# Optimization experiments

Hardware: AMD Instinct MI355X
Metric: run time of the kernel (lower is better)

The kernel has to match this reference:

```python
import jax, jax.numpy as jnp
import numpy as np

T, B, D, H = 2048, 64, 512, 512

def setup_inputs() -> dict:
    key = jax.random.key(0)
    ks = jax.random.split(key, 5)
    scale = 1.0 / np.sqrt(D + H)  # ~ torch Linear init scale
    inputs = jax.random.normal(ks[0], (T, B, D), dtype=jnp.float32)
    Wf = jax.random.normal(ks[1], (D + H, H), dtype=jnp.float32) * scale
    Wi = jax.random.normal(ks[2], (D + H, H), dtype=jnp.float32) * scale
    Wg = jax.random.normal(ks[3], (D + H, H), dtype=jnp.float32) * scale
    Wo = jax.random.normal(ks[4], (D + H, H), dtype=jnp.float32) * scale
    z = jnp.zeros((H,), dtype=jnp.float32)
    return {"inputs": inputs, "Wf": Wf, "bf": z, "Wi": Wi, "bi": z,
            "Wg": Wg, "bg": z, "Wo": Wo, "bo": z}

def reference(inputs, Wf, bf, Wi, bi, Wg, bg, Wo, bo):
    # Fuse the 4 gate GEMMs into one [D+H, 4H] matmul per step (same math).
    W = jnp.concatenate([Wf, Wi, Wg, Wo], axis=1)          # [D+H, 4H]
    b = jnp.concatenate([bf, bi, bg, bo], axis=0)          # [4H]
    Hdim = Wf.shape[1]
    Bsz = inputs.shape[1]
    h0 = jnp.zeros((Bsz, Hdim), dtype=inputs.dtype)
    c0 = jnp.zeros((Bsz, Hdim), dtype=inputs.dtype)

    def step(carry, x):
        hx, cx = carry
        combined = jnp.concatenate([x, hx], axis=1)        # [B, D+H]
        gates = combined @ W + b                           # [B, 4H]
        f, i, g, o = jnp.split(gates, 4, axis=1)
        f = jax.nn.sigmoid(f)
        i = jax.nn.sigmoid(i)
        g = jnp.tanh(g)
        o = jax.nn.sigmoid(o)
        cx = f * cx + i * g
        hx = o * jnp.tanh(cx)
        return (hx, cx), hx

    (hT, cT), stacked = jax.lax.scan(step, (h0, c0), inputs)
    return stacked, (hT, cT)
```

## Files before the change

### kernel.cpp

```cpp
#include <hip/hip_runtime.h>
#include <hip/hip_bf16.h>


#define T_N 2048
#define B_N 64
#define D_N 512
#define H_N 512
#define NBLK 64
#define NHEAT 192
#define CPB 8
#define GCPB 32
#define NTHR 256

#define STACK_ELEMS ((size_t)T_N * B_N * H_N)
#define HT_OFF STACK_ELEMS
#define CT_OFF (STACK_ELEMS + (size_t)B_N * H_N)

#define WS_DONE 0
#define WS_FLAGS 1024
#define WS_MIRROR 32768
#define WS_XB 262144

typedef __attribute__((ext_vector_type(4))) float f32x4;
typedef __attribute__((ext_vector_type(8))) short bf16x8;

__device__ __forceinline__ unsigned short f2bf(float f) {
  union { __hip_bfloat16 h; unsigned short u; } u;
  u.h = __float2bfloat16(f);
  return u.u;
}
__device__ __forceinline__ float bf2f(unsigned short us) {
  union { unsigned u32; float f; } x;
  x.u32 = ((unsigned)us) << 16;
  return x.f;
}
__device__ __forceinline__ float sigf(float x) { return 1.0f / (1.0f + __expf(-x)); }
__device__ __forceinline__ float tanhfast(float x) { return 1.0f - 2.0f / (__expf(2.0f * x) + 1.0f); }

__global__ void init_ws_kernel(unsigned* ws32) {
  int i = blockIdx.x * blockDim.x + threadIdx.x;
  if (i < 65536) ws32[i] = 0u;
}

__global__ void xconv_kernel(const float* __restrict__ X, unsigned short* __restrict__ Xb) {
  size_t i = ((size_t)blockIdx.x * blockDim.x + threadIdx.x) * 8;
  float4 v0 = *(const float4*)(X + i);
  float4 v1 = *(const float4*)(X + i + 4);
  bf16x8 o;
  o[0] = (short)f2bf(v0.x); o[1] = (short)f2bf(v0.y);
  o[2] = (short)f2bf(v0.z); o[3] = (short)f2bf(v0.w);
  o[4] = (short)f2bf(v1.x); o[5] = (short)f2bf(v1.y);
  o[6] = (short)f2bf(v1.z); o[7] = (short)f2bf(v1.w);
  *(bf16x8*)(Xb + i) = o;
}

__device__ __forceinline__ void load_x_tile(const unsigned short* Xb, const float* X,
                                            int t, int arow, int kg, bf16x8 (&xa)[16]) {
  if (Xb) {
    const unsigned short* xp = Xb + ((size_t)t * B_N + arow) * D_N + kg;
#pragma unroll
    for (int kk = 0; kk < 16; ++kk) xa[kk] = *(const bf16x8*)(xp + kk * 32);
  } else {
    const float* xp = X + ((size_t)t * B_N + arow) * D_N + kg;
#pragma unroll
    for (int kk = 0; kk < 16; ++kk) {
      float4 v0 = *(const float4*)(xp + kk * 32);
      float4 v1 = *(const float4*)(xp + kk * 32 + 4);
      bf16x8 a;
      a[0] = (short)f2bf(v0.x); a[1] = (short)f2bf(v0.y);
      a[2] = (short)f2bf(v0.z); a[3] = (short)f2bf(v0.w);
      a[4] = (short)f2bf(v1.x); a[5] = (short)f2bf(v1.y);
      a[6] = (short)f2bf(v1.z); a[7] = (short)f2bf(v1.w);
      xa[kk] = a;
    }
  }
}

__global__ __launch_bounds__(NTHR, 1) void lstm_kernel(
    const float* __restrict__ X, const unsigned short* __restrict__ Xb,
    const float* __restrict__ Wf, const float* __restrict__ bF,
    const float* __restrict__ Wi, const float* __restrict__ bI,
    const float* __restrict__ Wg, const float* __restrict__ bG,
    const float* __restrict__ Wo, const float* __restrict__ bO,
    unsigned char* wsb, float* __restrict__ out) {
  __shared__ unsigned short Wl[GCPB * (D_N + H_N)];
  __shared__ unsigned sReady;
  __shared__ int hstop;

  const int tid = threadIdx.x;
  const int blk = blockIdx.x;
  const int lane = tid & 63;

  if (blk >= NBLK) {
    if (tid == 0) *(volatile int*)&hstop = 0;
    __syncthreads();
    const unsigned* dp = (const unsigned*)(wsb + WS_DONE);
    float a = 1.0f + (float)(blk * NTHR + tid) * 1e-7f;
    const float hm = 0.99993f, hc = 1e-8f;
    for (long i = 0;; ++i) {
#pragma unroll
      for (int j = 0; j < 512; ++j) a = __builtin_fmaf(a, hm, hc);
      if (tid == 0 && (i & 63) == 0) {
        unsigned d = __hip_atomic_load(dp, __ATOMIC_RELAXED, __HIP_MEMORY_SCOPE_AGENT);
        if (d >= (unsigned)NBLK) *(volatile int*)&hstop = 1;
      }
      if (*(volatile int*)&hstop) break;
      if (i > (1l << 21)) break;
    }
    asm volatile("" :: "v"(a));
    return;
  }

  const int c0 = blk * CPB;
  const int w = tid >> 6;
  const int l16 = lane & 15;
  const int g16 = lane >> 4;
  const int cc = l16 & 7;
  const bool lo = (l16 < 8);

  if (tid == 0) *(volatile unsigned*)&sReady = 0u;

  for (int idx = tid; idx < GCPB * (D_N + H_N); idx += NTHR) {
    int k = idx >> 5;
    int cl = idx & 31;
    const float* wsrc = (cl < 8) ? Wf : (cl < 16) ? Wi : (cl < 24) ? Wg : Wo;
    float v = wsrc[(size_t)k * H_N + c0 + (cl & 7)];
    int pos = ((k >> 5) * 1024) + ((cl >> 4) * 512) + (((k >> 3) & 3) * 128) + ((cl & 15) * 8) + (k & 7);
    Wl[pos] = f2bf(v);
  }
  const float bias0 = lo ? bF[c0 + cc] : bI[c0 + cc];
  const float bias1 = lo ? bG[c0 + cc] : bO[c0 + cc];
  __syncthreads();

  const int arow = 16 * w + l16;
  const int kg = 8 * g16;
  const int lofs8 = lane * 8;
  const bool owner = (arow == blk);

  bf16x8 wb0[32], wb1[32];
#pragma unroll
  for (int K = 0; K < 32; ++K) {
    wb0[K] = *(const bf16x8*)&Wl[K * 1024 + lofs8];
    wb1[K] = *(const bf16x8*)&Wl[K * 1024 + 512 + lofs8];
  }

  unsigned* flags = (unsigned*)(wsb + WS_FLAGS);
  float cst[4] = {0.f, 0.f, 0.f, 0.f};
  float hT_local[4] = {0.f, 0.f, 0.f, 0.f};

  bf16x8 xa[16];
  load_x_tile(Xb, X, 0, arow, kg, xa);

  for (int t = 0; t < T_N; ++t) {
    const int slotR = (t + 1) & 1;
    const int slotW = t & 1;

    f32x4 x0a = {0,0,0,0}, x0b = {0,0,0,0}, x1a = {0,0,0,0}, x1b = {0,0,0,0};
#pragma unroll
    for (int kk = 0; kk < 8; ++kk) {
      x0a = __builtin_amdgcn_mfma_f32_16x16x32_bf16(xa[kk], wb0[kk], x0a, 0, 0, 0);
      x1a = __builtin_amdgcn_mfma_f32_16x16x32_bf16(xa[kk], wb1[kk], x1a, 0, 0, 0);
    }
#pragma unroll
    for (int kk = 8; kk < 16; ++kk) {
      x0b = __builtin_amdgcn_mfma_f32_16x16x32_bf16(xa[kk], wb0[kk], x0b, 0, 0, 0);
      x1b = __builtin_amdgcn_mfma_f32_16x16x32_bf16(xa[kk], wb1[kk], x1b, 0, 0, 0);
    }

    if (t > 0) {
      const unsigned tgt = (unsigned)t;
      if (w == 0) {
        long guard = 0;
        for (;;) {
          unsigned fv = __hip_atomic_load(flags + lane, __ATOMIC_RELAXED, __HIP_MEMORY_SCOPE_AGENT);
          if (__all((int)(fv >= tgt))) break;
          if (++guard > 2) __builtin_amdgcn_s_sleep(8);
          if (guard > (1l << 16)) break;
        }
        if (lane == 0) *(volatile unsigned*)&sReady = tgt;
      } else {
        long guard = 0;
        while (*(volatile unsigned*)&sReady < tgt) {
          if (++guard > (1l << 22)) break;
        }
      }
    }

    unsigned long long hq0[16], hq1[16];
    {
      const unsigned long long* hbase =
          (const unsigned long long*)(wsb + WS_MIRROR + (size_t)slotR * 65536);
#pragma unroll
      for (int kk = 0; kk < 16; ++kk) {
        const unsigned long long* hp = hbase + (size_t)(g16 + 4 * kk) * 128 + arow * 2;
        hq0[kk] = __hip_atomic_load(hp, __ATOMIC_RELAXED, __HIP_MEMORY_SCOPE_AGENT);
        hq1[kk] = __hip_atomic_load(hp + 1, __ATOMIC_RELAXED, __HIP_MEMORY_SCOPE_AGENT);
      }
    }

    f32x4 h0a = {0,0,0,0}, h0b = {0,0,0,0}, h1a = {0,0,0,0}, h1b = {0,0,0,0};
#pragma unroll
    for (int kk = 0; kk < 8; ++kk) {
      union { unsigned long long q[2]; bf16x8 v; } u;
      u.q[0] = hq0[kk]; u.q[1] = hq1[kk];
      h0a = __builtin_amdgcn_mfma_f32_16x16x32_bf16(u.v, wb0[16 + kk], h0a, 0, 0, 0);
      h1a = __builtin_amdgcn_mfma_f32_16x16x32_bf16(u.v, wb1[16 + kk], h1a, 0, 0, 0);
    }
#pragma unroll
    for (int kk = 8; kk < 16; ++kk) {
      union { unsigned long long q[2]; bf16x8 v; } u;
      u.q[0] = hq0[kk]; u.q[1] = hq1[kk];
      h0b = __builtin_amdgcn_mfma_f32_16x16x32_bf16(u.v, wb0[16 + kk], h0b, 0, 0, 0);
      h1b = __builtin_amdgcn_mfma_f32_16x16x32_bf16(u.v, wb1[16 + kk], h1b, 0, 0, 0);
    }
    f32x4 m0v = (x0a + x0b) + (h0a + h0b);
    f32x4 m1v = (x1a + x1b) + (h1a + h1b);

    float hv[4];
#pragma unroll
    for (int r = 0; r < 4; ++r) {
      float m0 = m0v[r] + bias0;
      float m1 = m1v[r] + bias1;
      float p0 = __shfl_xor(m0, 8, 64);
      float p1 = __shfl_xor(m1, 8, 64);
      float fv = lo ? m0 : p0;
      float iv = lo ? p0 : m0;
      float gv = lo ? m1 : p1;
      float ov = lo ? p1 : m1;
      float f = sigf(fv), i = sigf(iv), g = tanhfast(gv), o = sigf(ov);
      float c = f * cst[r] + i * g;
      cst[r] = c;
      hv[r] = o * tanhfast(c);
    }

    {
      unsigned* rb = (unsigned*)(wsb + WS_MIRROR + (size_t)slotW * 65536) + blk * 256;
#pragma unroll
      for (int r = 0; r < 4; ++r) {
        int row = 16 * w + 4 * g16 + r;
        unsigned short hb = f2bf(hv[r]);
        unsigned opp = __shfl_xor((unsigned)hb, 1, 64);
        if (lo && (cc & 1) == 0) {
          unsigned pack = (unsigned)hb | (opp << 16);
          __hip_atomic_store(rb + row * 4 + (cc >> 1), pack,
                             __ATOMIC_RELAXED, __HIP_MEMORY_SCOPE_AGENT);
        }
      }
    }

    asm volatile("s_waitcnt vmcnt(0)" ::: "memory");
    __syncthreads();
    if (tid == 0) {
      __hip_atomic_store(flags + blk, (unsigned)(t + 1),
                         __ATOMIC_RELAXED, __HIP_MEMORY_SCOPE_AGENT);
    }

    if (t + 1 < T_N) load_x_tile(Xb, X, t + 1, arow, kg, xa);

    if (owner && t > 0) {
      float* oprev = out + (size_t)(t - 1) * (B_N * H_N) + (size_t)blk * H_N + kg;
#pragma unroll
      for (int kk = 0; kk < 16; ++kk) {
        union { unsigned long long q[2]; bf16x8 v; } u;
        u.q[0] = hq0[kk]; u.q[1] = hq1[kk];
        float4 f0, f1;
        f0.x = bf2f((unsigned short)u.v[0]); f0.y = bf2f((unsigned short)u.v[1]);
        f0.z = bf2f((unsigned short)u.v[2]); f0.w = bf2f((unsigned short)u.v[3]);
        f1.x = bf2f((unsigned short)u.v[4]); f1.y = bf2f((unsigned short)u.v[5]);
        f1.z = bf2f((unsigned short)u.v[6]); f1.w = bf2f((unsigned short)u.v[7]);
        *(float4*)(oprev + kk * 32) = f0;
        *(float4*)(oprev + kk * 32 + 4) = f1;
      }
    }

    if (t == T_N - 1) {
      float* obase = out + (size_t)t * (B_N * H_N);
#pragma unroll
      for (int r = 0; r < 4; ++r) {
        int row = 16 * w + 4 * g16 + r;
        if (lo) obase[(size_t)row * H_N + c0 + cc] = hv[r];
        hT_local[r] = hv[r];
      }
    }
  }

  if (lo) {
#pragma unroll
    for (int r = 0; r < 4; ++r) {
      int row = 16 * w + 4 * g16 + r;
      out[HT_OFF + (size_t)row * H_N + c0 + cc] = hT_local[r];
      out[CT_OFF + (size_t)row * H_N + c0 + cc] = cst[r];
    }
  }
  __syncthreads();
  if (tid == 0)
    __hip_atomic_fetch_add((unsigned*)(wsb + WS_DONE), 1u,
                           __ATOMIC_RELAXED, __HIP_MEMORY_SCOPE_AGENT);
}

extern "C" void kernel_launch(void* const* d_in, const int* in_sizes, int n_in,
                              void* d_out, int out_size, void* d_ws, size_t ws_size,
                              hipStream_t stream) {
  const float* X  = (const float*)d_in[0];
  const float* Wf = (const float*)d_in[1];
  const float* bF = (const float*)d_in[2];
  const float* Wi = (const float*)d_in[3];
  const float* bI = (const float*)d_in[4];
  const float* Wg = (const float*)d_in[5];
  const float* bG = (const float*)d_in[6];
  const float* Wo = (const float*)d_in[7];
  const float* bO = (const float*)d_in[8];
  float* out = (float*)d_out;

  unsigned char* ws = (unsigned char*)d_ws;
  const size_t need_xb = WS_XB + (size_t)T_N * B_N * D_N * 2;
  unsigned short* Xb = (ws_size >= need_xb) ? (unsigned short*)(ws + WS_XB) : nullptr;

  init_ws_kernel<<<dim3(256), dim3(256), 0, stream>>>((unsigned*)ws);
  if (Xb) {
    xconv_kernel<<<dim3((T_N * B_N * D_N) / 8 / 256), dim3(256), 0, stream>>>(X, Xb);
  }
  lstm_kernel<<<dim3(NBLK + NHEAT), dim3(NTHR), 0, stream>>>(
      X, Xb, Wf, bF, Wi, bI, Wg, bG, Wo, bO, ws, out);
}
```

Baseline: 10.72 ms.

## Halve persistent LSTM blocks to 32 with 512 threads covering two column slices

Each persistent block now runs 8 waves split into two 8-column gate slices, so only 32 blocks take part in the per-step all-to-all flag barrier instead of 64. The hidden-state exchange buffer is relaid as a per-block 16-column ring with matching read addressing, and the output-owner mapping is adjusted to match. The spin-wait sleeps are shortened and the guard limits raised. Fewer participants should cut barrier latency per timestep, at the cost of doubling per-CU register and MFMA work per block and adding more intra-block synchronisation.

Result: slower. 38.03 ms (+254.9%).

```diff
diff --git a/kernel.cpp b/kernel.cpp
--- a/kernel.cpp
+++ b/kernel.cpp
@@ -6,11 +6,10 @@
 #define B_N 64
 #define D_N 512
 #define H_N 512
-#define NBLK 64
-#define NHEAT 192
-#define CPB 8
-#define GCPB 32
-#define NTHR 256
+#define NBLK 32
+#define NHEAT 224
+#define NTHR 512
+#define BH (B_N * H_N)
 
 #define STACK_ELEMS ((size_t)T_N * B_N * H_N)
 #define HT_OFF STACK_ELEMS
@@ -18,7 +17,7 @@
 
 #define WS_DONE 0
 #define WS_FLAGS 1024
-#define WS_MIRROR 32768
+#define WS_RING 32768
 #define WS_XB 262144
 
 typedef __attribute__((ext_vector_type(4))) float f32x4;
@@ -83,7 +82,7 @@
     const float* __restrict__ Wg, const float* __restrict__ bG,
     const float* __restrict__ Wo, const float* __restrict__ bO,
     unsigned char* wsb, float* __restrict__ out) {
-  __shared__ unsigned short Wl[GCPB * (D_N + H_N)];
+  __shared__ unsigned short Wl[32768];
   __shared__ unsigned sReady;
   __shared__ int hstop;
 
@@ -111,8 +110,9 @@
     return;
   }
 
-  const int c0 = blk * CPB;
   const int w = tid >> 6;
+  const int cs = w >> 2;
+  const int m = w & 3;
   const int l16 = lane & 15;
   const int g16 = lane >> 4;
   const int cc = l16 & 7;
@@ -120,29 +120,34 @@
 
   if (tid == 0) *(volatile unsigned*)&sReady = 0u;
 
-  for (int idx = tid; idx < GCPB * (D_N + H_N); idx += NTHR) {
-    int k = idx >> 5;
-    int cl = idx & 31;
-    const float* wsrc = (cl < 8) ? Wf : (cl < 16) ? Wi : (cl < 24) ? Wg : Wo;
-    float v = wsrc[(size_t)k * H_N + c0 + (cl & 7)];
-    int pos = ((k >> 5) * 1024) + ((cl >> 4) * 512) + (((k >> 3) & 3) * 128) + ((cl & 15) * 8) + (k & 7);
-    Wl[pos] = f2bf(v);
-  }
-  const float bias0 = lo ? bF[c0 + cc] : bI[c0 + cc];
-  const float bias1 = lo ? bG[c0 + cc] : bO[c0 + cc];
-  __syncthreads();
-
-  const int arow = 16 * w + l16;
+  bf16x8 wb0[32], wb1[32];
+  for (int p = 0; p < 2; ++p) {
+    __syncthreads();
+    for (int idx = tid; idx < 32768; idx += NTHR) {
+      int k = idx >> 5;
+      int cl = idx & 31;
+      const float* wsrc = (cl < 8) ? Wf : (cl < 16) ? Wi : (cl < 24) ? Wg : Wo;
+      float v = wsrc[(size_t)k * H_N + 16 * blk + 8 * p + (cl & 7)];
+      int pos = ((k >> 5) * 1024) + ((cl >> 4) * 512) + (((k >> 3) & 3) * 128) + ((cl & 15) * 8) + (k & 7);
+      Wl[pos] = f2bf(v);
+    }
+    __syncthreads();
+    if (cs == p) {
+#pragma unroll
+      for (int K = 0; K < 32; ++K) {
+        wb0[K] = *(const bf16x8*)&Wl[K * 1024 + lane * 8];
+        wb1[K] = *(const bf16x8*)&Wl[K * 1024 + 512 + lane * 8];
+      }
+    }
+  }
+
+  const int c0w = 16 * blk + 8 * cs;
+  const float bias0 = lo ? bF[c0w + cc] : bI[c0w + cc];
+  const float bias1 = lo ? bG[c0w + cc] : bO[c0w + cc];
+
+  const int arow = 16 * m + l16;
   const int kg = 8 * g16;
-  const int lofs8 = lane * 8;
-  const bool owner = (arow == blk);
-
-  bf16x8 wb0[32], wb1[32];
-#pragma unroll
-  for (int K = 0; K < 32; ++K) {
-    wb0[K] = *(const bf16x8*)&Wl[K * 1024 + lofs8];
-    wb1[K] = *(const bf16x8*)&Wl[K * 1024 + 512 + lofs8];
-  }
+  const bool owner = (cs == 0) && ((arow >> 1) == blk);
 
   unsigned* flags = (unsigned*)(wsb + WS_FLAGS);
   float cst[4] = {0.f, 0.f, 0.f, 0.f};
@@ -172,27 +177,28 @@
       if (w == 0) {
         long guard = 0;
         for (;;) {
-          unsigned fv = __hip_atomic_load(flags + lane, __ATOMIC_RELAXED, __HIP_MEMORY_SCOPE_AGENT);
+          unsigned fv = __hip_atomic_load(flags + (lane & 31), __ATOMIC_RELAXED, __HIP_MEMORY_SCOPE_AGENT);
           if (__all((int)(fv >= tgt))) break;
-          if (++guard > 2) __builtin_amdgcn_s_sleep(8);
-          if (guard > (1l << 16)) break;
+          if (++guard > 4) __builtin_amdgcn_s_sleep(2);
+          if (guard > (1l << 18)) break;
         }
         if (lane == 0) *(volatile unsigned*)&sReady = tgt;
       } else {
         long guard = 0;
         while (*(volatile unsigned*)&sReady < tgt) {
-          if (++guard > (1l << 22)) break;
+          if (++guard > (1l << 24)) break;
         }
       }
     }
 
     unsigned long long hq0[16], hq1[16];
     {
-      const unsigned long long* hbase =
-          (const unsigned long long*)(wsb + WS_MIRROR + (size_t)slotR * 65536);
+      const unsigned char* hb = wsb + WS_RING + (size_t)slotR * 65536;
+      const unsigned char* hrow = hb + arow * 32 + (g16 & 1) * 16;
 #pragma unroll
       for (int kk = 0; kk < 16; ++kk) {
-        const unsigned long long* hp = hbase + (size_t)(g16 + 4 * kk) * 128 + arow * 2;
+        const unsigned long long* hp =
+            (const unsigned long long*)(hrow + (size_t)(2 * kk + (g16 >> 1)) * 2048);
         hq0[kk] = __hip_atomic_load(hp, __ATOMIC_RELAXED, __HIP_MEMORY_SCOPE_AGENT);
         hq1[kk] = __hip_atomic_load(hp + 1, __ATOMIC_RELAXED, __HIP_MEMORY_SCOPE_AGENT);
       }
@@ -234,15 +240,15 @@
     }
 
     {
-      unsigned* rb = (unsigned*)(wsb + WS_MIRROR + (size_t)slotW * 65536) + blk * 256;
+      unsigned char* rb = wsb + WS_RING + (size_t)slotW * 65536 + (size_t)blk * 2048;
 #pragma unroll
       for (int r = 0; r < 4; ++r) {
-        int row = 16 * w + 4 * g16 + r;
-        unsigned short hb = f2bf(hv[r]);
-        unsigned opp = __shfl_xor((unsigned)hb, 1, 64);
+        int row = 16 * m + 4 * g16 + r;
+        unsigned short hb16 = f2bf(hv[r]);
+        unsigned opp = __shfl_xor((unsigned)hb16, 1, 64);
         if (lo && (cc & 1) == 0) {
-          unsigned pack = (unsigned)hb | (opp << 16);
-          __hip_atomic_store(rb + row * 4 + (cc >> 1), pack,
+          unsigned pack = (unsigned)hb16 | (opp << 16);
+          __hip_atomic_store((unsigned*)(rb + row * 32 + (8 * cs + cc) * 2), pack,
                              __ATOMIC_RELAXED, __HIP_MEMORY_SCOPE_AGENT);
         }
       }
@@ -258,7 +264,7 @@
     if (t + 1 < T_N) load_x_tile(Xb, X, t + 1, arow, kg, xa);
 
     if (owner && t > 0) {
-      float* oprev = out + (size_t)(t - 1) * (B_N * H_N) + (size_t)blk * H_N + kg;
+      float* oprev = out + (size_t)(t - 1) * BH + (size_t)arow * H_N + kg;
 #pragma unroll
       for (int kk = 0; kk < 16; ++kk) {
         union { unsigned long long q[2]; bf16x8 v; } u;
@@ -274,11 +280,11 @@
     }
 
     if (t == T_N - 1) {
-      float* obase = out + (size_t)t * (B_N * H_N);
+      float* obase = out + (size_t)t * BH;
 #pragma unroll
       for (int r = 0; r < 4; ++r) {
-        int row = 16 * w + 4 * g16 + r;
-        if (lo) obase[(size_t)row * H_N + c0 + cc] = hv[r];
+        int row = 16 * m + 4 * g16 + r;
+        if (lo) obase[(size_t)row * H_N + c0w + cc] = hv[r];
         hT_local[r] = hv[r];
       }
     }
@@ -287,9 +293,9 @@
   if (lo) {
 #pragma unroll
     for (int r = 0; r < 4; ++r) {
-      int row = 16 * w + 4 * g16 + r;
-      out[HT_OFF + (size_t)row * H_N + c0 + cc] = hT_local[r];
-      out[CT_OFF + (size_t)row * H_N + c0 + cc] = cst[r];
+      int row = 16 * m + 4 * g16 + r;
+      out[HT_OFF + (size_t)row * H_N + c0w + cc] = hT_local[r];
+      out[CT_OFF + (size_t)row * H_N + c0w + cc] = cst[r];
     }
   }
   __syncthreads();
```

## Tag hidden-state ring entries with step index for per-chunk readiness polling

Applied to the files above, without the earlier changes.

Each stored hidden value now carries the step number in its upper 16 bits, doubling the ring buffer size. Readers check these tags on each chunk and overlap the recurrent MFMAs with incremental loads, instead of waiting on a full per-step write drain. The producer's vmcnt wait and __syncthreads are replaced by a bare s_barrier, and the output write for the previous step is folded into the read loop. The trade-off is twice the data traffic per h read and extra tag checks, and the flag wait still exists alongside the tags.

Result: slower. 20.53 ms (+91.6%).

```diff
diff --git a/kernel.cpp b/kernel.cpp
--- a/kernel.cpp
+++ b/kernel.cpp
@@ -11,6 +11,7 @@
 #define CPB 8
 #define GCPB 32
 #define NTHR 256
+#define BH (B_N * H_N)
 
 #define STACK_ELEMS ((size_t)T_N * B_N * H_N)
 #define HT_OFF STACK_ELEMS
@@ -18,8 +19,9 @@
 
 #define WS_DONE 0
 #define WS_FLAGS 1024
-#define WS_MIRROR 32768
-#define WS_XB 262144
+#define WS_RING 32768
+#define WS_XB 524288
+#define RING_SLOT_U32 32768
 
 typedef __attribute__((ext_vector_type(4))) float f32x4;
 typedef __attribute__((ext_vector_type(8))) short bf16x8;
@@ -29,9 +31,9 @@
   u.h = __float2bfloat16(f);
   return u.u;
 }
-__device__ __forceinline__ float bf2f(unsigned short us) {
+__device__ __forceinline__ float u2f(unsigned u) {
   union { unsigned u32; float f; } x;
-  x.u32 = ((unsigned)us) << 16;
+  x.u32 = u;
   return x.f;
 }
 __device__ __forceinline__ float sigf(float x) { return 1.0f / (1.0f + __expf(-x)); }
@@ -39,7 +41,7 @@
 
 __global__ void init_ws_kernel(unsigned* ws32) {
   int i = blockIdx.x * blockDim.x + threadIdx.x;
-  if (i < 65536) ws32[i] = 0u;
+  if (i < 73728) ws32[i] = 0u;
 }
 
 __global__ void xconv_kernel(const float* __restrict__ X, unsigned short* __restrict__ Xb) {
@@ -111,6 +113,7 @@
     return;
   }
 
+  unsigned* ring32 = (unsigned*)(wsb + WS_RING);
   const int c0 = blk * CPB;
   const int w = tid >> 6;
   const int l16 = lane & 15;
@@ -155,16 +158,16 @@
     const int slotR = (t + 1) & 1;
     const int slotW = t & 1;
 
-    f32x4 x0a = {0,0,0,0}, x0b = {0,0,0,0}, x1a = {0,0,0,0}, x1b = {0,0,0,0};
+    f32x4 a0a = {0,0,0,0}, a0b = {0,0,0,0}, a1a = {0,0,0,0}, a1b = {0,0,0,0};
 #pragma unroll
     for (int kk = 0; kk < 8; ++kk) {
-      x0a = __builtin_amdgcn_mfma_f32_16x16x32_bf16(xa[kk], wb0[kk], x0a, 0, 0, 0);
-      x1a = __builtin_amdgcn_mfma_f32_16x16x32_bf16(xa[kk], wb1[kk], x1a, 0, 0, 0);
+      a0a = __builtin_amdgcn_mfma_f32_16x16x32_bf16(xa[kk], wb0[kk], a0a, 0, 0, 0);
+      a1a = __builtin_amdgcn_mfma_f32_16x16x32_bf16(xa[kk], wb1[kk], a1a, 0, 0, 0);
     }
 #pragma unroll
     for (int kk = 8; kk < 16; ++kk) {
-      x0b = __builtin_amdgcn_mfma_f32_16x16x32_bf16(xa[kk], wb0[kk], x0b, 0, 0, 0);
-      x1b = __builtin_amdgcn_mfma_f32_16x16x32_bf16(xa[kk], wb1[kk], x1b, 0, 0, 0);
+      a0b = __builtin_amdgcn_mfma_f32_16x16x32_bf16(xa[kk], wb0[kk], a0b, 0, 0, 0);
+      a1b = __builtin_amdgcn_mfma_f32_16x16x32_bf16(xa[kk], wb1[kk], a1b, 0, 0, 0);
     }
 
     if (t > 0) {
@@ -174,47 +177,89 @@
         for (;;) {
           unsigned fv = __hip_atomic_load(flags + lane, __ATOMIC_RELAXED, __HIP_MEMORY_SCOPE_AGENT);
           if (__all((int)(fv >= tgt))) break;
-          if (++guard > 2) __builtin_amdgcn_s_sleep(8);
+          if (++guard > 2) __builtin_amdgcn_s_sleep(2);
           if (guard > (1l << 16)) break;
         }
         if (lane == 0) *(volatile unsigned*)&sReady = tgt;
       } else {
         long guard = 0;
         while (*(volatile unsigned*)&sReady < tgt) {
-          if (++guard > (1l << 22)) break;
-        }
-      }
-    }
-
-    unsigned long long hq0[16], hq1[16];
+          if (++guard > (1l << 24)) break;
+        }
+      }
+    }
+
     {
-      const unsigned long long* hbase =
-          (const unsigned long long*)(wsb + WS_MIRROR + (size_t)slotR * 65536);
+      const unsigned tag = (unsigned)t;
+      const unsigned long long pat =
+          ((unsigned long long)tag << 16) | ((unsigned long long)tag << 48);
+      const unsigned long long msk = 0xFFFF0000FFFF0000ull;
+      const unsigned long long* rbase =
+          (const unsigned long long*)(ring32 + (size_t)slotR * RING_SLOT_U32) + (size_t)arow * 4;
+      float* oprev = out + (size_t)(t - 1) * BH + (size_t)blk * H_N + kg;
+      const bool wout = owner && (t > 0);
+
+      unsigned long long q[8][4];
+#pragma unroll
+      for (int kk = 0; kk < 8; ++kk) {
+        const unsigned long long* bp = rbase + (size_t)(4 * kk + g16) * 256;
+        q[kk][0] = __hip_atomic_load(bp + 0, __ATOMIC_RELAXED, __HIP_MEMORY_SCOPE_AGENT);
+        q[kk][1] = __hip_atomic_load(bp + 1, __ATOMIC_RELAXED, __HIP_MEMORY_SCOPE_AGENT);
+        q[kk][2] = __hip_atomic_load(bp + 2, __ATOMIC_RELAXED, __HIP_MEMORY_SCOPE_AGENT);
+        q[kk][3] = __hip_atomic_load(bp + 3, __ATOMIC_RELAXED, __HIP_MEMORY_SCOPE_AGENT);
+      }
 #pragma unroll
       for (int kk = 0; kk < 16; ++kk) {
-        const unsigned long long* hp = hbase + (size_t)(g16 + 4 * kk) * 128 + arow * 2;
-        hq0[kk] = __hip_atomic_load(hp, __ATOMIC_RELAXED, __HIP_MEMORY_SCOPE_AGENT);
-        hq1[kk] = __hip_atomic_load(hp + 1, __ATOMIC_RELAXED, __HIP_MEMORY_SCOPE_AGENT);
-      }
-    }
-
-    f32x4 h0a = {0,0,0,0}, h0b = {0,0,0,0}, h1a = {0,0,0,0}, h1b = {0,0,0,0};
-#pragma unroll
-    for (int kk = 0; kk < 8; ++kk) {
-      union { unsigned long long q[2]; bf16x8 v; } u;
-      u.q[0] = hq0[kk]; u.q[1] = hq1[kk];
-      h0a = __builtin_amdgcn_mfma_f32_16x16x32_bf16(u.v, wb0[16 + kk], h0a, 0, 0, 0);
-      h1a = __builtin_amdgcn_mfma_f32_16x16x32_bf16(u.v, wb1[16 + kk], h1a, 0, 0, 0);
-    }
-#pragma unroll
-    for (int kk = 8; kk < 16; ++kk) {
-      union { unsigned long long q[2]; bf16x8 v; } u;
-      u.q[0] = hq0[kk]; u.q[1] = hq1[kk];
-      h0b = __builtin_amdgcn_mfma_f32_16x16x32_bf16(u.v, wb0[16 + kk], h0b, 0, 0, 0);
-      h1b = __builtin_amdgcn_mfma_f32_16x16x32_bf16(u.v, wb1[16 + kk], h1b, 0, 0, 0);
-    }
-    f32x4 m0v = (x0a + x0b) + (h0a + h0b);
-    f32x4 m1v = (x1a + x1b) + (h1a + h1b);
+        const int s = kk & 7;
+        const unsigned long long* bp = rbase + (size_t)(4 * kk + g16) * 256;
+        {
+          long guard = 0;
+          for (;;) {
+            unsigned long long st = ((q[s][0] ^ pat) | (q[s][1] ^ pat) |
+                                     (q[s][2] ^ pat) | (q[s][3] ^ pat)) & msk;
+            if (!__any((int)(st != 0ull))) break;
+            __builtin_amdgcn_s_sleep(1);
+            q[s][0] = __hip_atomic_load(bp + 0, __ATOMIC_RELAXED, __HIP_MEMORY_SCOPE_AGENT);
+            q[s][1] = __hip_atomic_load(bp + 1, __ATOMIC_RELAXED, __HIP_MEMORY_SCOPE_AGENT);
+            q[s][2] = __hip_atomic_load(bp + 2, __ATOMIC_RELAXED, __HIP_MEMORY_SCOPE_AGENT);
+            q[s][3] = __hip_atomic_load(bp + 3, __ATOMIC_RELAXED, __HIP_MEMORY_SCOPE_AGENT);
+            if (++guard > 256) break;
+          }
+        }
+        union { unsigned u[4]; bf16x8 v; } f;
+#pragma unroll
+        for (int m2 = 0; m2 < 4; ++m2) {
+          unsigned lo32 = (unsigned)q[s][m2];
+          unsigned hi32 = (unsigned)(q[s][m2] >> 32);
+          f.u[m2] = (lo32 & 0xFFFFu) | (hi32 << 16);
+        }
+        if (wout) {
+          float4 f0, f1;
+          f0.x = u2f((unsigned)q[s][0] << 16); f0.y = u2f((unsigned)(q[s][0] >> 32) << 16);
+          f0.z = u2f((unsigned)q[s][1] << 16); f0.w = u2f((unsigned)(q[s][1] >> 32) << 16);
+          f1.x = u2f((unsigned)q[s][2] << 16); f1.y = u2f((unsigned)(q[s][2] >> 32) << 16);
+          f1.z = u2f((unsigned)q[s][3] << 16); f1.w = u2f((unsigned)(q[s][3] >> 32) << 16);
+          *(float4*)(oprev + kk * 32) = f0;
+          *(float4*)(oprev + kk * 32 + 4) = f1;
+        }
+        if (kk < 8) {
+          a0a = __builtin_amdgcn_mfma_f32_16x16x32_bf16(f.v, wb0[16 + kk], a0a, 0, 0, 0);
+          a1a = __builtin_amdgcn_mfma_f32_16x16x32_bf16(f.v, wb1[16 + kk], a1a, 0, 0, 0);
+        } else {
+          a0b = __builtin_amdgcn_mfma_f32_16x16x32_bf16(f.v, wb0[16 + kk], a0b, 0, 0, 0);
+          a1b = __builtin_amdgcn_mfma_f32_16x16x32_bf16(f.v, wb1[16 + kk], a1b, 0, 0, 0);
+        }
+        if (kk < 8) {
+          const unsigned long long* np = rbase + (size_t)(4 * (kk + 8) + g16) * 256;
+          q[s][0] = __hip_atomic_load(np + 0, __ATOMIC_RELAXED, __HIP_MEMORY_SCOPE_AGENT);
+          q[s][1] = __hip_atomic_load(np + 1, __ATOMIC_RELAXED, __HIP_MEMORY_SCOPE_AGENT);
+          q[s][2] = __hip_atomic_load(np + 2, __ATOMIC_RELAXED, __HIP_MEMORY_SCOPE_AGENT);
+          q[s][3] = __hip_atomic_load(np + 3, __ATOMIC_RELAXED, __HIP_MEMORY_SCOPE_AGENT);
+        }
+      }
+    }
+    f32x4 m0v = a0a + a0b;
+    f32x4 m1v = a1a + a1b;
 
     float hv[4];
 #pragma unroll
@@ -234,22 +279,24 @@
     }
 
     {
-      unsigned* rb = (unsigned*)(wsb + WS_MIRROR + (size_t)slotW * 65536) + blk * 256;
+      unsigned* wbase = ring32 + (size_t)slotW * RING_SLOT_U32 + blk * 512;
+      const unsigned tagw = ((unsigned)(t + 1)) << 16;
 #pragma unroll
       for (int r = 0; r < 4; ++r) {
         int row = 16 * w + 4 * g16 + r;
         unsigned short hb = f2bf(hv[r]);
         unsigned opp = __shfl_xor((unsigned)hb, 1, 64);
-        if (lo && (cc & 1) == 0) {
-          unsigned pack = (unsigned)hb | (opp << 16);
-          __hip_atomic_store(rb + row * 4 + (cc >> 1), pack,
+        bool mine = ((cc & 1) == 0) && (lo ? (r < 2) : (r >= 2));
+        if (mine) {
+          unsigned long long rv = ((unsigned long long)((unsigned)hb | tagw)) |
+                                  (((unsigned long long)(opp | tagw)) << 32);
+          __hip_atomic_store((unsigned long long*)(wbase + row * 8 + cc), rv,
                              __ATOMIC_RELAXED, __HIP_MEMORY_SCOPE_AGENT);
         }
       }
     }
-
-    asm volatile("s_waitcnt vmcnt(0)" ::: "memory");
-    __syncthreads();
+    asm volatile("" ::: "memory");
+    __builtin_amdgcn_s_barrier();
     if (tid == 0) {
       __hip_atomic_store(flags + blk, (unsigned)(t + 1),
                          __ATOMIC_RELAXED, __HIP_MEMORY_SCOPE_AGENT);
@@ -257,24 +304,8 @@
 
     if (t + 1 < T_N) load_x_tile(Xb, X, t + 1, arow, kg, xa);
 
-    if (owner && t > 0) {
-      float* oprev = out + (size_t)(t - 1) * (B_N * H_N) + (size_t)blk * H_N + kg;
-#pragma unroll
-      for (int kk = 0; kk < 16; ++kk) {
-        union { unsigned long long q[2]; bf16x8 v; } u;
-        u.q[0] = hq0[kk]; u.q[1] = hq1[kk];
-        float4 f0, f1;
-        f0.x = bf2f((unsigned short)u.v[0]); f0.y = bf2f((unsigned short)u.v[1]);
-        f0.z = bf2f((unsigned short)u.v[2]); f0.w = bf2f((unsigned short)u.v[3]);
-        f1.x = bf2f((unsigned short)u.v[4]); f1.y = bf2f((unsigned short)u.v[5]);
-        f1.z = bf2f((unsigned short)u.v[6]); f1.w = bf2f((unsigned short)u.v[7]);
-        *(float4*)(oprev + kk * 32) = f0;
-        *(float4*)(oprev + kk * 32 + 4) = f1;
-      }
-    }
-
     if (t == T_N - 1) {
-      float* obase = out + (size_t)t * (B_N * H_N);
+      float* obase = out + (size_t)t * BH;
 #pragma unroll
       for (int r = 0; r < 4; ++r) {
         int row = 16 * w + 4 * g16 + r;
@@ -316,7 +347,7 @@
   const size_t need_xb = WS_XB + (size_t)T_N * B_N * D_N * 2;
   unsigned short* Xb = (ws_size >= need_xb) ? (unsigned short*)(ws + WS_XB) : nullptr;
 
-  init_ws_kernel<<<dim3(256), dim3(256), 0, stream>>>((unsigned*)ws);
+  init_ws_kernel<<<dim3(512), dim3(256), 0, stream>>>((unsigned*)ws);
   if (Xb) {
     xconv_kernel<<<dim3((T_N * B_N * D_N) / 8 / 256), dim3(256), 0, stream>>>(X, Xb);
   }
```

## Replace block-level flag barrier with per-wave flags and incremental readiness polling

Applied to the files above, without the earlier changes.

Each wave now publishes its own per-step flag and polls the 64 producer flags for its row slice directly, so the __syncthreads and shared-memory ready broadcast go away. Hidden-state chunks are loaded as soon as the four producer blocks feeding that chunk are ready, so early loads overlap with waiting on later producers. The cost is four times as many flag slots and more polling traffic from all waves. The per-wave correctness depends on each wave only needing rows written by matching waves in other blocks.

Result: slower. 11.44 ms (+6.7%).

```diff
diff --git a/kernel.cpp b/kernel.cpp
--- a/kernel.cpp
+++ b/kernel.cpp
@@ -11,6 +11,7 @@
 #define CPB 8
 #define GCPB 32
 #define NTHR 256
+#define BH (B_N * H_N)
 
 #define STACK_ELEMS ((size_t)T_N * B_N * H_N)
 #define HT_OFF STACK_ELEMS
@@ -84,7 +85,6 @@
     const float* __restrict__ Wo, const float* __restrict__ bO,
     unsigned char* wsb, float* __restrict__ out) {
   __shared__ unsigned short Wl[GCPB * (D_N + H_N)];
-  __shared__ unsigned sReady;
   __shared__ int hstop;
 
   const int tid = threadIdx.x;
@@ -118,8 +118,6 @@
   const int cc = l16 & 7;
   const bool lo = (l16 < 8);
 
-  if (tid == 0) *(volatile unsigned*)&sReady = 0u;
-
   for (int idx = tid; idx < GCPB * (D_N + H_N); idx += NTHR) {
     int k = idx >> 5;
     int cl = idx & 31;
@@ -145,6 +143,8 @@
   }
 
   unsigned* flags = (unsigned*)(wsb + WS_FLAGS);
+  unsigned* myflag = flags + w * 64 + blk;
+  const unsigned* pollp = flags + w * 64 + lane;
   float cst[4] = {0.f, 0.f, 0.f, 0.f};
   float hT_local[4] = {0.f, 0.f, 0.f, 0.f};
 
@@ -165,36 +165,37 @@
     for (int kk = 8; kk < 16; ++kk) {
       x0b = __builtin_amdgcn_mfma_f32_16x16x32_bf16(xa[kk], wb0[kk], x0b, 0, 0, 0);
       x1b = __builtin_amdgcn_mfma_f32_16x16x32_bf16(xa[kk], wb1[kk], x1b, 0, 0, 0);
-    }
-
-    if (t > 0) {
-      const unsigned tgt = (unsigned)t;
-      if (w == 0) {
-        long guard = 0;
-        for (;;) {
-          unsigned fv = __hip_atomic_load(flags + lane, __ATOMIC_RELAXED, __HIP_MEMORY_SCOPE_AGENT);
-          if (__all((int)(fv >= tgt))) break;
-          if (++guard > 2) __builtin_amdgcn_s_sleep(8);
-          if (guard > (1l << 16)) break;
-        }
-        if (lane == 0) *(volatile unsigned*)&sReady = tgt;
-      } else {
-        long guard = 0;
-        while (*(volatile unsigned*)&sReady < tgt) {
-          if (++guard > (1l << 22)) break;
-        }
-      }
     }
 
     unsigned long long hq0[16], hq1[16];
     {
       const unsigned long long* hbase =
           (const unsigned long long*)(wsb + WS_MIRROR + (size_t)slotR * 65536);
-#pragma unroll
-      for (int kk = 0; kk < 16; ++kk) {
-        const unsigned long long* hp = hbase + (size_t)(g16 + 4 * kk) * 128 + arow * 2;
-        hq0[kk] = __hip_atomic_load(hp, __ATOMIC_RELAXED, __HIP_MEMORY_SCOPE_AGENT);
-        hq1[kk] = __hip_atomic_load(hp + 1, __ATOMIC_RELAXED, __HIP_MEMORY_SCOPE_AGENT);
+      unsigned long long rdy = ~0ull;
+      if (t > 0) {
+        const unsigned tgt = (unsigned)t;
+        unsigned fv = __hip_atomic_load(pollp, __ATOMIC_RELAXED, __HIP_MEMORY_SCOPE_AGENT);
+        rdy = __ballot((int)(fv >= tgt));
+        long guard = 0;
+#pragma unroll
+        for (int kk = 0; kk < 16; ++kk) {
+          while (((rdy >> (4 * kk)) & 0xFull) != 0xFull) {
+            if (++guard > 2) __builtin_amdgcn_s_sleep(1);
+            fv = __hip_atomic_load(pollp, __ATOMIC_RELAXED, __HIP_MEMORY_SCOPE_AGENT);
+            rdy = __ballot((int)(fv >= tgt));
+            if (guard > (1l << 18)) { rdy = ~0ull; break; }
+          }
+          const unsigned long long* hp = hbase + (size_t)(g16 + 4 * kk) * 128 + arow * 2;
+          hq0[kk] = __hip_atomic_load(hp, __ATOMIC_RELAXED, __HIP_MEMORY_SCOPE_AGENT);
+          hq1[kk] = __hip_atomic_load(hp + 1, __ATOMIC_RELAXED, __HIP_MEMORY_SCOPE_AGENT);
+        }
+      } else {
+#pragma unroll
+        for (int kk = 0; kk < 16; ++kk) {
+          const unsigned long long* hp = hbase + (size_t)(g16 + 4 * kk) * 128 + arow * 2;
+          hq0[kk] = __hip_atomic_load(hp, __ATOMIC_RELAXED, __HIP_MEMORY_SCOPE_AGENT);
+          hq1[kk] = __hip_atomic_load(hp + 1, __ATOMIC_RELAXED, __HIP_MEMORY_SCOPE_AGENT);
+        }
       }
     }
 
@@ -249,16 +250,15 @@
     }
 
     asm volatile("s_waitcnt vmcnt(0)" ::: "memory");
-    __syncthreads();
-    if (tid == 0) {
-      __hip_atomic_store(flags + blk, (unsigned)(t + 1),
+    if (lane == 0) {
+      __hip_atomic_store(myflag, (unsigned)(t + 1),
                          __ATOMIC_RELAXED, __HIP_MEMORY_SCOPE_AGENT);
     }
 
     if (t + 1 < T_N) load_x_tile(Xb, X, t + 1, arow, kg, xa);
 
     if (owner && t > 0) {
-      float* oprev = out + (size_t)(t - 1) * (B_N * H_N) + (size_t)blk * H_N + kg;
+      float* oprev = out + (size_t)(t - 1) * BH + (size_t)blk * H_N + kg;
 #pragma unroll
       for (int kk = 0; kk < 16; ++kk) {
         union { unsigned long long q[2]; bf16x8 v; } u;
@@ -274,7 +274,7 @@
     }
 
     if (t == T_N - 1) {
-      float* obase = out + (size_t)t * (B_N * H_N);
+      float* obase = out + (size_t)t * BH;
 #pragma unroll
       for (int r = 0; r < 4; ++r) {
         int row = 16 * w + 4 * g16 + r;
```
